# Performance work log

Measured on AMD Instinct MI355X. Metric: run time of the kernel, lower is better.

Reference implementation:

```python
import jax, jax.numpy as jnp
import numpy as np

D_MODEL = 1024
NHEAD = 16
HEAD_DIM = D_MODEL // NHEAD
NEG = -1e9
LN_EPS = 1e-5


def setup_inputs() -> dict:
    key = jax.random.key(0)
    ks = jax.random.split(key, 12)
    B, S, D = 2, 2048, D_MODEL
    scale = 1.0 / np.sqrt(D)
    inp = {
        "x": jax.random.normal(ks[0], (B, S, D), jnp.float32),
        "mask": jax.random.randint(ks[1], (B, S), 0, 2, jnp.int32),
        "wq": jax.random.normal(ks[2], (D, D), jnp.float32) * scale,
        "bq": jnp.zeros((D,), jnp.float32),
        "wk": jax.random.normal(ks[3], (D, D), jnp.float32) * scale,
        "bk": jnp.zeros((D,), jnp.float32),
        "wv": jax.random.normal(ks[4], (D, D), jnp.float32) * scale,
        "bv": jnp.zeros((D,), jnp.float32),
        "wo": jax.random.normal(ks[5], (D, D), jnp.float32) * scale,
        "bo": jnp.zeros((D,), jnp.float32),
        "attn_bias": jax.random.normal(ks[6], (1, NHEAD, 1, 1), jnp.float32) * 0.02,
        "ln_g": jnp.ones((D,), jnp.float32),
        "ln_b": jnp.zeros((D,), jnp.float32),
    }
    return inp


def _layer_norm(x, g, b):
    mu = jnp.mean(x, axis=-1, keepdims=True)
    var = jnp.var(x, axis=-1, keepdims=True)
    return (x - mu) * jax.lax.rsqrt(var + LN_EPS) * g + b


def reference(x, mask, wq, bq, wk, bk, wv, bv, wo, bo, attn_bias, ln_g, ln_b):
    B, S, D = x.shape
    H, Hd = NHEAD, HEAD_DIM
    # QKV projections -> [B, H, S, Hd]
    q = (x @ wq + bq).reshape(B, S, H, Hd).transpose(0, 2, 1, 3)
    k = (x @ wk + bk).reshape(B, S, H, Hd).transpose(0, 2, 1, 3)
    v = (x @ wv + bv).reshape(B, S, H, Hd).transpose(0, 2, 1, 3)
    # Scores [B, H, S, S] with per-head scalar bias
    scores = jnp.einsum("bhsd,bhtd->bhst", q, k) / jnp.sqrt(jnp.float32(Hd))
    scores = scores + attn_bias
    # mask [B,S] -> [B,1,1,S]; masked_fill where mask == 0
    m = (mask[:, None, None, :] == 0)
    scores = jnp.where(m, jnp.float32(NEG), scores)
    attn = jax.nn.softmax(scores, axis=-1)  # dropout = identity (eval)
    out = jnp.einsum("bhst,bhtd->bhsd", attn, v)
    out = out.transpose(0, 2, 1, 3).reshape(B, S, D)
    out = out @ wo + bo
    return _layer_norm(x + out, ln_g, ln_b)
```

## Files before the change

kernel.cpp:

```cpp
#include <hip/hip_runtime.h>

typedef __attribute__((ext_vector_type(8))) short short8;
typedef __attribute__((ext_vector_type(4))) float f32x4;
typedef __attribute__((ext_vector_type(16))) float f32x16;
typedef __attribute__((ext_vector_type(4))) unsigned short us4;

#define DEV __device__ __forceinline__

#define GLD16(gp, lp) __builtin_amdgcn_global_load_lds( \
    (const __attribute__((address_space(1))) void*)(gp), \
    (__attribute__((address_space(3))) void*)(lp), 16, 0, 0)

DEV unsigned short f2bf(float f) {
    union { float f; unsigned u; } v; v.f = f;
    unsigned r = v.u + 0x7fffu + ((v.u >> 16) & 1u);
    return (unsigned short)(r >> 16);
}

DEV float bf2f(unsigned short u) {
    union { unsigned u; float f; } v; v.u = (unsigned)u << 16;
    return v.f;
}

DEV unsigned cvtpk(float lo, float hi) {
    unsigned r;
    asm("v_cvt_pk_bf16_f32 %0, %1, %2" : "=v"(r) : "v"(lo), "v"(hi));
    return r;
}

DEV float fexp2(float x) {
#if __has_builtin(__builtin_amdgcn_exp2f)
    return __builtin_amdgcn_exp2f(x);
#else
    return __expf(x * 0.69314718056f);
#endif
}

__global__ __launch_bounds__(256) void k_transw(const float* __restrict__ wq, const float* __restrict__ wk,
                                                const float* __restrict__ wv, const float* __restrict__ wo,
                                                unsigned short* __restrict__ wt) {
    __shared__ float tile[32][33];
    const int z = blockIdx.z;
    const float* src = (z == 0) ? wq : (z == 1) ? wk : (z == 2) ? wv : wo;
    unsigned short* dst = wt + (size_t)z * (1u << 20);
    const int n0 = blockIdx.x * 32, k0 = blockIdx.y * 32;
    const int tx = threadIdx.x, ty = threadIdx.y;
#pragma unroll
    for (int i = 0; i < 4; ++i)
        tile[ty + i * 8][tx] = src[(size_t)(k0 + ty + i * 8) * 1024 + n0 + tx];
    __syncthreads();
#pragma unroll
    for (int i = 0; i < 4; ++i)
        dst[(size_t)(n0 + ty + i * 8) * 1024 + k0 + tx] = f2bf(tile[tx][ty + i * 8]);
}

__global__ __launch_bounds__(256) void k_gemm_qkv(const float* __restrict__ X,
                                                  const unsigned short* __restrict__ Wt,
                                                  const float* __restrict__ bq,
                                                  const float* __restrict__ bk,
                                                  const float* __restrict__ bv,
                                                  const int* __restrict__ mask,
                                                  unsigned short* __restrict__ Qo,
                                                  unsigned short* __restrict__ Ko,
                                                  unsigned short* __restrict__ Vo,
                                                  float qscale) {
    __shared__ unsigned short lA[2][128 * 32];
    __shared__ unsigned short lB[2][3][64 * 32];
    const int m0 = blockIdx.y * 128, n0 = blockIdx.x * 64;
    const int tid = threadIdx.x;
    const int lane = tid & 63;
    const int w = tid >> 6, wm = w >> 1, wn = w & 1;

    const int arow0 = tid >> 2, acl = tid & 3;
    const int arow1 = (tid + 256) >> 2;
    const int brow = tid >> 2;
    const float* agp0 = X + (size_t)(m0 + arow0) * 1024 + acl * 8;
    const float* agp1 = X + (size_t)(m0 + arow1) * 1024 + acl * 8;
    const unsigned short* bgp[3];
#pragma unroll
    for (int z = 0; z < 3; ++z)
        bgp[z] = Wt + ((size_t)z << 20) + (size_t)(n0 + brow) * 1024 + acl * 8;
    const int apc0 = ((arow0 << 2) | (acl ^ ((arow0 >> 1) & 3))) * 8;
    const int apc1 = ((arow1 << 2) | (acl ^ ((arow1 >> 1) & 3))) * 8;
    const int bpc  = ((brow  << 2) | (acl ^ ((brow  >> 1) & 3))) * 8;

    int ach[4], bch[2];
#pragma unroll
    for (int mt = 0; mt < 4; ++mt) {
        int row = wm * 64 + mt * 16 + (lane & 15);
        ach[mt] = ((row << 2) | ((lane >> 4) ^ ((row >> 1) & 3))) * 8;
    }
#pragma unroll
    for (int nt = 0; nt < 2; ++nt) {
        int row = wn * 32 + nt * 16 + (lane & 15);
        bch[nt] = ((row << 2) | ((lane >> 4) ^ ((row >> 1) & 3))) * 8;
    }

    f32x4 acc[3][4][2] = {};
    float4 ra0l = *(const float4*)agp0, ra0h = *(const float4*)(agp0 + 4);
    float4 ra1l = *(const float4*)agp1, ra1h = *(const float4*)(agp1 + 4);
    short8 rb[3];
#pragma unroll
    for (int z = 0; z < 3; ++z) rb[z] = *(const short8*)bgp[z];

    for (int t = 0; t < 32; ++t) {
        unsigned short* sA = lA[t & 1];
        union { unsigned u[4]; short8 s8; } p0, p1;
        p0.u[0] = cvtpk(ra0l.x, ra0l.y); p0.u[1] = cvtpk(ra0l.z, ra0l.w);
        p0.u[2] = cvtpk(ra0h.x, ra0h.y); p0.u[3] = cvtpk(ra0h.z, ra0h.w);
        p1.u[0] = cvtpk(ra1l.x, ra1l.y); p1.u[1] = cvtpk(ra1l.z, ra1l.w);
        p1.u[2] = cvtpk(ra1h.x, ra1h.y); p1.u[3] = cvtpk(ra1h.z, ra1h.w);
        *(short8*)(sA + apc0) = p0.s8;
        *(short8*)(sA + apc1) = p1.s8;
#pragma unroll
        for (int z = 0; z < 3; ++z)
            *(short8*)(lB[t & 1][z] + bpc) = rb[z];
        if (t < 31) {
            ra0l = *(const float4*)(agp0 + (t + 1) * 32);
            ra0h = *(const float4*)(agp0 + (t + 1) * 32 + 4);
            ra1l = *(const float4*)(agp1 + (t + 1) * 32);
            ra1h = *(const float4*)(agp1 + (t + 1) * 32 + 4);
#pragma unroll
            for (int z = 0; z < 3; ++z) rb[z] = *(const short8*)(bgp[z] + (t + 1) * 32);
        }
        __syncthreads();
        short8 af[4], bf[3][2];
#pragma unroll
        for (int mt = 0; mt < 4; ++mt) af[mt] = *(const short8*)(sA + ach[mt]);
#pragma unroll
        for (int z = 0; z < 3; ++z)
#pragma unroll
            for (int nt = 0; nt < 2; ++nt) bf[z][nt] = *(const short8*)(lB[t & 1][z] + bch[nt]);
#pragma unroll
        for (int z = 0; z < 3; ++z)
#pragma unroll
            for (int mt = 0; mt < 4; ++mt)
#pragma unroll
                for (int nt = 0; nt < 2; ++nt)
                    acc[z][mt][nt] = __builtin_amdgcn_mfma_f32_16x16x32_bf16(af[mt], bf[z][nt], acc[z][mt][nt], 0, 0, 0);
    }

#pragma unroll
    for (int z = 0; z < 3; ++z) {
        const float* bias = (z == 0) ? bq : (z == 1) ? bk : bv;
        const float scl = (z == 0) ? qscale : 1.0f;
        unsigned short* outp = (z == 0) ? Qo : (z == 1) ? Ko : Vo;
#pragma unroll
        for (int nt = 0; nt < 2; ++nt) {
            const int col = n0 + wn * 32 + nt * 16 + (lane & 15);
            const float bvv = bias[col];
            const int h = col >> 6, hd = col & 63;
#pragma unroll
            for (int mt = 0; mt < 4; ++mt) {
#pragma unroll
                for (int r = 0; r < 4; ++r) {
                    const int row = m0 + wm * 64 + mt * 16 + (lane >> 4) * 4 + r;
                    const int b = row >> 11, s = row & 2047;
                    float v = (acc[z][mt][nt][r] + bvv) * scl;
                    if (z == 2) {
                        v *= (mask[(size_t)b * 2048 + s] ? 1.0f : 0.0f);
                        outp[(size_t)((b * 16 + h) * 64 + hd) * 2048 + s] = f2bf(v);
                    } else {
                        outp[(size_t)((b * 16 + h) * 2048 + s) * 64 + hd] = f2bf(v);
                    }
                }
            }
        }
    }
}

__global__ __launch_bounds__(256) void k_gemm_o(const unsigned short* __restrict__ A,
                                                const unsigned short* __restrict__ Wt,
                                                const float* __restrict__ bias,
                                                unsigned short* __restrict__ out) {
    __shared__ unsigned short lA[2][128 * 32];
    __shared__ unsigned short lB[2][64 * 32];
    const int m0 = blockIdx.y * 128, n0 = blockIdx.x * 64;
    const int tid = threadIdx.x;
    const int lane = tid & 63;
    const int w = tid >> 6, wm = w >> 1, wn = w & 1;

    const int arow0 = tid >> 2, acl = tid & 3;
    const int arow1 = (tid + 256) >> 2;
    const int brow = tid >> 2;
    const unsigned short* agp0 = A + (size_t)(m0 + arow0) * 1024 + acl * 8;
    const unsigned short* agp1 = A + (size_t)(m0 + arow1) * 1024 + acl * 8;
    const unsigned short* bgp  = Wt + (size_t)(n0 + brow) * 1024 + acl * 8;
    const int apc0 = ((arow0 << 2) | (acl ^ ((arow0 >> 1) & 3))) * 8;
    const int apc1 = ((arow1 << 2) | (acl ^ ((arow1 >> 1) & 3))) * 8;
    const int bpc  = ((brow  << 2) | (acl ^ ((brow  >> 1) & 3))) * 8;

    int ach[4], bch[2];
#pragma unroll
    for (int mt = 0; mt < 4; ++mt) {
        int row = wm * 64 + mt * 16 + (lane & 15);
        ach[mt] = ((row << 2) | ((lane >> 4) ^ ((row >> 1) & 3))) * 8;
    }
#pragma unroll
    for (int nt = 0; nt < 2; ++nt) {
        int row = wn * 32 + nt * 16 + (lane & 15);
        bch[nt] = ((row << 2) | ((lane >> 4) ^ ((row >> 1) & 3))) * 8;
    }

    f32x4 acc[4][2] = {};
    short8 ra0 = *(const short8*)agp0;
    short8 ra1 = *(const short8*)agp1;
    short8 rb0 = *(const short8*)bgp;

    for (int t = 0; t < 32; ++t) {
        unsigned short* sA = lA[t & 1];
        unsigned short* sB = lB[t & 1];
        *(short8*)(sA + apc0) = ra0;
        *(short8*)(sA + apc1) = ra1;
        *(short8*)(sB + bpc)  = rb0;
        if (t < 31) {
            ra0 = *(const short8*)(agp0 + (t + 1) * 32);
            ra1 = *(const short8*)(agp1 + (t + 1) * 32);
            rb0 = *(const short8*)(bgp  + (t + 1) * 32);
        }
        __syncthreads();
        short8 af[4], bf[2];
#pragma unroll
        for (int mt = 0; mt < 4; ++mt) af[mt] = *(const short8*)(sA + ach[mt]);
#pragma unroll
        for (int nt = 0; nt < 2; ++nt) bf[nt] = *(const short8*)(sB + bch[nt]);
#pragma unroll
        for (int mt = 0; mt < 4; ++mt)
#pragma unroll
            for (int nt = 0; nt < 2; ++nt)
                acc[mt][nt] = __builtin_amdgcn_mfma_f32_16x16x32_bf16(af[mt], bf[nt], acc[mt][nt], 0, 0, 0);
    }

#pragma unroll
    for (int nt = 0; nt < 2; ++nt) {
        const int col = n0 + wn * 32 + nt * 16 + (lane & 15);
        const float bv = bias[col];
#pragma unroll
        for (int mt = 0; mt < 4; ++mt)
#pragma unroll
            for (int r = 0; r < 4; ++r) {
                const int row = m0 + wm * 64 + mt * 16 + (lane >> 4) * 4 + r;
                out[(size_t)row * 1024 + col] = f2bf(acc[mt][nt][r] + bv);
            }
    }
}

__global__ __launch_bounds__(256, 2) void k_attn(const unsigned short* __restrict__ Qb,
                                                 const unsigned short* __restrict__ Kb,
                                                 const unsigned short* __restrict__ Vt,
                                                 const int* __restrict__ mask,
                                                 unsigned short* __restrict__ po0,
                                                 unsigned short* __restrict__ po1,
                                                 float* __restrict__ lp0,
                                                 float* __restrict__ lp1) {
    __shared__ unsigned short ksm[2 * 4096];
    __shared__ unsigned short vsm[2 * 4096];
    __shared__ unsigned short mv[1024];
    const int id = blockIdx.x;
    const int xcd = id & 7, slot = id >> 3;
    const int half = slot & 1, qt = (slot >> 1) & 7, bh = xcd * 4 + (slot >> 4);
    const int b = bh >> 4, h = bh & 15;
    const int tid = threadIdx.x, l = tid & 63, w = tid >> 6;
    const int q = l & 31, hi = l >> 5;

    {
        int4 m = ((const int4*)(mask + b * 2048 + half * 1024))[tid];
        us4 mb = { (unsigned short)(m.x ? 0x3F80 : 0), (unsigned short)(m.y ? 0x3F80 : 0),
                   (unsigned short)(m.z ? 0x3F80 : 0), (unsigned short)(m.w ? 0x3F80 : 0) };
        ((us4*)mv)[tid] = mb;
    }
    asm volatile("s_waitcnt lgkmcnt(0)" ::: "memory");

    const size_t bhS = (size_t)bh * 2048;
    const unsigned short* Kbh = Kb + (bhS + half * 1024) * 64;
    const unsigned short* Vbh = Vt + (size_t)bh * 64 * 2048;
    const int q0 = qt * 256 + w * 64;

    const int srow = l >> 3;
    const int sxor = 8 * ((l & 7) ^ ((l >> 3) & 7));
    const unsigned short* Ksrc = Kbh + (size_t)(w * 16 + srow) * 64 + sxor;
    const unsigned short* Vsrc = Vbh + (size_t)(w * 16 + srow) * 2048 + half * 1024 + sxor;
    unsigned short* lk0 = ksm + w * 1024;
    unsigned short* lv0 = vsm + w * 1024;

#define STAGE(kt_, buf_) { \
    const unsigned short* gk = Ksrc + (size_t)(kt_) * 4096; \
    const unsigned short* gv = Vsrc + (kt_) * 64; \
    unsigned short* lk = lk0 + (buf_) * 4096; \
    unsigned short* lv = lv0 + (buf_) * 4096; \
    GLD16(gk, lk); GLD16(gk + 512, lk + 512); \
    GLD16(gv, lv); GLD16(gv + 16384, lv + 512); }

    int kro[2][4], vro[2][2][2];
#pragma unroll
    for (int sub = 0; sub < 2; ++sub) {
#pragma unroll
        for (int db = 0; db < 4; ++db) {
            int key = q + sub * 32;
            kro[sub][db] = key * 128 + ((db * 32 + hi * 16) ^ ((key & 7) << 4));
        }
#pragma unroll
        for (int kg = 0; kg < 2; ++kg)
#pragma unroll
            for (int dh = 0; dh < 2; ++dh) {
                int row = q + dh * 32;
                vro[sub][kg][dh] = row * 128 + ((sub * 64 + kg * 32 + hi * 16) ^ ((row & 7) << 4));
            }
    }

    short8 qfA[4], qfB[4];
#pragma unroll
    for (int db = 0; db < 4; ++db) {
        qfA[db] = *(const short8*)(Qb + (bhS + q0 + q) * 64 + db * 16 + hi * 8);
        qfB[db] = *(const short8*)(Qb + (bhS + q0 + 32 + q) * 64 + db * 16 + hi * 8);
    }

    f32x16 o00 = {}, o01 = {}, o10 = {}, o11 = {}, ol0 = {}, ol1 = {};

    STAGE(0, 0);

    for (int kt = 0; kt < 16; ++kt) {
        const int cur = kt & 1;
        if (kt < 15) {
            STAGE(kt + 1, cur ^ 1);
            asm volatile("s_waitcnt vmcnt(4)" ::: "memory");
        } else {
            asm volatile("s_waitcnt vmcnt(0)" ::: "memory");
        }
        __builtin_amdgcn_s_barrier();
        __builtin_amdgcn_sched_barrier(0);
        const char* kb = (const char*)(ksm + cur * 4096);
        const char* vb = (const char*)(vsm + cur * 4096);
#pragma unroll
        for (int sub = 0; sub < 2; ++sub) {
            short8 kf0 = *(const short8*)(kb + kro[sub][0]);
            short8 kf1 = *(const short8*)(kb + kro[sub][1]);
            short8 kf2 = *(const short8*)(kb + kro[sub][2]);
            short8 kf3 = *(const short8*)(kb + kro[sub][3]);
            f32x16 sa0 = {}, sa1 = {};
            __builtin_amdgcn_s_setprio(1);
            sa0 = __builtin_amdgcn_mfma_f32_32x32x16_bf16(kf0, qfA[0], sa0, 0, 0, 0);
            sa1 = __builtin_amdgcn_mfma_f32_32x32x16_bf16(kf0, qfB[0], sa1, 0, 0, 0);
            sa0 = __builtin_amdgcn_mfma_f32_32x32x16_bf16(kf1, qfA[1], sa0, 0, 0, 0);
            sa1 = __builtin_amdgcn_mfma_f32_32x32x16_bf16(kf1, qfB[1], sa1, 0, 0, 0);
            sa0 = __builtin_amdgcn_mfma_f32_32x32x16_bf16(kf2, qfA[2], sa0, 0, 0, 0);
            sa1 = __builtin_amdgcn_mfma_f32_32x32x16_bf16(kf2, qfB[2], sa1, 0, 0, 0);
            sa0 = __builtin_amdgcn_mfma_f32_32x32x16_bf16(kf3, qfA[3], sa0, 0, 0, 0);
            sa1 = __builtin_amdgcn_mfma_f32_32x32x16_bf16(kf3, qfB[3], sa1, 0, 0, 0);
            __builtin_amdgcn_s_setprio(0);
            union { unsigned u[4]; short8 s8; } afA[2], afB[2];
            {
                float p[16];
#pragma unroll
                for (int r = 0; r < 16; ++r) p[r] = fexp2(sa0[r]);
#pragma unroll
                for (int kg = 0; kg < 2; ++kg) {
                    unsigned P0 = cvtpk(p[kg * 8 + 0], p[kg * 8 + 1]);
                    unsigned P1 = cvtpk(p[kg * 8 + 2], p[kg * 8 + 3]);
                    unsigned P2 = cvtpk(p[kg * 8 + 4], p[kg * 8 + 5]);
                    unsigned P3 = cvtpk(p[kg * 8 + 6], p[kg * 8 + 7]);
                    asm("v_permlane32_swap_b32 %0, %1" : "+v"(P0), "+v"(P2));
                    asm("v_permlane32_swap_b32 %0, %1" : "+v"(P1), "+v"(P3));
                    afA[kg].u[0] = P0; afA[kg].u[1] = P1; afA[kg].u[2] = P2; afA[kg].u[3] = P3;
                }
            }
            {
                float p[16];
#pragma unroll
                for (int r = 0; r < 16; ++r) p[r] = fexp2(sa1[r]);
#pragma unroll
                for (int kg = 0; kg < 2; ++kg) {
                    unsigned P0 = cvtpk(p[kg * 8 + 0], p[kg * 8 + 1]);
                    unsigned P1 = cvtpk(p[kg * 8 + 2], p[kg * 8 + 3]);
                    unsigned P2 = cvtpk(p[kg * 8 + 4], p[kg * 8 + 5]);
                    unsigned P3 = cvtpk(p[kg * 8 + 6], p[kg * 8 + 7]);
                    asm("v_permlane32_swap_b32 %0, %1" : "+v"(P0), "+v"(P2));
                    asm("v_permlane32_swap_b32 %0, %1" : "+v"(P1), "+v"(P3));
                    afB[kg].u[0] = P0; afB[kg].u[1] = P1; afB[kg].u[2] = P2; afB[kg].u[3] = P3;
                }
            }
#pragma unroll
            for (int kg = 0; kg < 2; ++kg) {
                short8 vf0 = *(const short8*)(vb + vro[sub][kg][0]);
                short8 vf1 = *(const short8*)(vb + vro[sub][kg][1]);
                short8 mfr = *(const short8*)(mv + kt * 64 + sub * 32 + kg * 16 + hi * 8);
                __builtin_amdgcn_s_setprio(1);
                o00 = __builtin_amdgcn_mfma_f32_32x32x16_bf16(afA[kg].s8, vf0, o00, 0, 0, 0);
                o01 = __builtin_amdgcn_mfma_f32_32x32x16_bf16(afA[kg].s8, vf1, o01, 0, 0, 0);
                o10 = __builtin_amdgcn_mfma_f32_32x32x16_bf16(afB[kg].s8, vf0, o10, 0, 0, 0);
                o11 = __builtin_amdgcn_mfma_f32_32x32x16_bf16(afB[kg].s8, vf1, o11, 0, 0, 0);
                ol0 = __builtin_amdgcn_mfma_f32_32x32x16_bf16(afA[kg].s8, mfr, ol0, 0, 0, 0);
                ol1 = __builtin_amdgcn_mfma_f32_32x32x16_bf16(afB[kg].s8, mfr, ol1, 0, 0, 0);
                __builtin_amdgcn_s_setprio(0);
            }
        }
        __builtin_amdgcn_sched_barrier(0);
        if (kt < 15) __builtin_amdgcn_s_barrier();
    }
#undef STAGE

    float* lpx = half ? lp1 : lp0;
    if (q == 0) {
#pragma unroll
        for (int r = 0; r < 16; ++r) {
            int crow = (r & 3) + 8 * (r >> 2) + 4 * hi;
            lpx[bhS + q0 + crow] = ol0[r];
            lpx[bhS + q0 + 32 + crow] = ol1[r];
        }
    }
    unsigned short* popA = (half ? po1 : po0) + ((size_t)b * 2048 + q0) * 1024 + h * 64 + q;
    unsigned short* popB = popA + (size_t)32 * 1024;
#pragma unroll
    for (int r = 0; r < 16; ++r) {
        int qrow = (r & 3) + 8 * (r >> 2) + 4 * hi;
        popA[(size_t)qrow * 1024] = f2bf(o00[r]);
        popA[(size_t)qrow * 1024 + 32] = f2bf(o01[r]);
        popB[(size_t)qrow * 1024] = f2bf(o10[r]);
        popB[(size_t)qrow * 1024 + 32] = f2bf(o11[r]);
    }
}

__global__ __launch_bounds__(256) void k_comb(const unsigned short* __restrict__ po0,
                                              const unsigned short* __restrict__ po1,
                                              const float* __restrict__ lp0,
                                              const float* __restrict__ lp1,
                                              unsigned short* __restrict__ ao) {
    const int idx8 = blockIdx.x * 256 + threadIdx.x;
    const int e = idx8 * 8;
    const int row = e >> 10, c = e & 1023;
    const int h = c >> 6, b = row >> 11, s = row & 2047;
    const size_t li = ((size_t)(b * 16 + h) << 11) + s;
    const float rinv = __builtin_amdgcn_rcpf(lp0[li] + lp1[li]);
    short8 a0 = ((const short8*)po0)[idx8];
    short8 a1 = ((const short8*)po1)[idx8];
    short8 o;
#pragma unroll
    for (int j = 0; j < 8; ++j)
        o[j] = (short)f2bf((bf2f((unsigned short)a0[j]) + bf2f((unsigned short)a1[j])) * rinv);
    ((short8*)ao)[idx8] = o;
}

__global__ __launch_bounds__(256) void k_ln(const float* __restrict__ x, const unsigned short* __restrict__ op,
                                            const float* __restrict__ g, const float* __restrict__ be,
                                            float* __restrict__ out) {
    const int row = blockIdx.x, tid = threadIdx.x;
    const float4 xv = ((const float4*)(x + (size_t)row * 1024))[tid];
    const us4 ov = ((const us4*)(op + (size_t)row * 1024))[tid];
    float4 v = { xv.x + bf2f(ov.x), xv.y + bf2f(ov.y), xv.z + bf2f(ov.z), xv.w + bf2f(ov.w) };
    float sum = v.x + v.y + v.z + v.w;
    float ss = v.x * v.x + v.y * v.y + v.z * v.z + v.w * v.w;
#pragma unroll
    for (int xm = 1; xm < 64; xm <<= 1) {
        sum += __shfl_xor(sum, xm, 64);
        ss += __shfl_xor(ss, xm, 64);
    }
    __shared__ float red[8];
    const int lane = tid & 63, w = tid >> 6;
    if (lane == 0) { red[w] = sum; red[4 + w] = ss; }
    __syncthreads();
    sum = red[0] + red[1] + red[2] + red[3];
    ss = red[4] + red[5] + red[6] + red[7];
    const float mu = sum * (1.0f / 1024.0f);
    const float rstd = rsqrtf(ss * (1.0f / 1024.0f) - mu * mu + 1e-5f);
    const float4 gv = ((const float4*)g)[tid];
    const float4 bv = ((const float4*)be)[tid];
    float4 o = { (v.x - mu) * rstd * gv.x + bv.x, (v.y - mu) * rstd * gv.y + bv.y,
                 (v.z - mu) * rstd * gv.z + bv.z, (v.w - mu) * rstd * gv.w + bv.w };
    ((float4*)(out + (size_t)row * 1024))[tid] = o;
}

extern "C" void kernel_launch(void* const* d_in, const int* in_sizes, int n_in,
                              void* d_out, int out_size, void* d_ws, size_t ws_size,
                              hipStream_t stream) {
    const float* x        = (const float*)d_in[0];
    const int*   mask     = (const int*)d_in[1];
    const float* wq       = (const float*)d_in[2];
    const float* bq       = (const float*)d_in[3];
    const float* wk       = (const float*)d_in[4];
    const float* bk       = (const float*)d_in[5];
    const float* wv       = (const float*)d_in[6];
    const float* bv       = (const float*)d_in[7];
    const float* wo       = (const float*)d_in[8];
    const float* bo       = (const float*)d_in[9];
    const float* ln_g     = (const float*)d_in[11];
    const float* ln_b     = (const float*)d_in[12];

    char* ws = (char*)d_ws;
    unsigned short* po0 = (unsigned short*)(ws);
    unsigned short* wt  = (unsigned short*)(ws + (8ll  << 20));
    unsigned short* qb  = (unsigned short*)(ws + (16ll << 20));
    unsigned short* kb  = (unsigned short*)(ws + (24ll << 20));
    unsigned short* vtb = (unsigned short*)(ws + (32ll << 20));
    unsigned short* po1 = (unsigned short*)(ws + (40ll << 20));
    float*          lp0 = (float*)(ws + (48ll << 20));
    float*          lp1 = (float*)(ws + (48ll << 20) + (256ll << 10));
    unsigned short* ao  = qb;
    unsigned short* opj = kb;

    const float qscale = 0.125f * 1.44269504f;

    k_transw<<<dim3(32, 32, 4), dim3(32, 8), 0, stream>>>(wq, wk, wv, wo, wt);
    k_gemm_qkv<<<dim3(16, 32), 256, 0, stream>>>(x, wt, bq, bk, bv, mask, qb, kb, vtb, qscale);
    k_attn<<<512, 256, 0, stream>>>(qb, kb, vtb, mask, po0, po1, lp0, lp1);
    k_comb<<<2048, 256, 0, stream>>>(po0, po1, lp0, lp1, ao);
    k_gemm_o<<<dim3(16, 32), 256, 0, stream>>>(ao, wt + (3u << 20), bo, opj);
    k_ln<<<4096, 256, 0, stream>>>(x, opj, ln_g, ln_b, (float*)d_out);
}
```

Measured before the change: 124.0 us.

## Pre-convert X to bf16, fuse split-attention combine into O-projection, swizzle GEMM blocks

New measurement: 132.1 us. 6.6% more time.

```diff
diff --git a/kernel.cpp b/kernel.cpp
--- a/kernel.cpp
+++ b/kernel.cpp
@@ -34,6 +34,14 @@
 #else
     return __expf(x * 0.69314718056f);
 #endif
+}
+
+__global__ __launch_bounds__(256) void k_convert(const float* __restrict__ x,
+                                                 unsigned short* __restrict__ xb) {
+    int i = blockIdx.x * 256 + threadIdx.x;
+    float4 v = ((const float4*)x)[i];
+    us4 o = { f2bf(v.x), f2bf(v.y), f2bf(v.z), f2bf(v.w) };
+    ((us4*)xb)[i] = o;
 }
 
 __global__ __launch_bounds__(256) void k_transw(const float* __restrict__ wq, const float* __restrict__ wk,
@@ -54,7 +62,7 @@
         dst[(size_t)(n0 + ty + i * 8) * 1024 + k0 + tx] = f2bf(tile[tx][ty + i * 8]);
 }
 
-__global__ __launch_bounds__(256) void k_gemm_qkv(const float* __restrict__ X,
+__global__ __launch_bounds__(256) void k_gemm_qkv(const unsigned short* __restrict__ A,
                                                   const unsigned short* __restrict__ Wt,
                                                   const float* __restrict__ bq,
                                                   const float* __restrict__ bk,
@@ -66,7 +74,9 @@
                                                   float qscale) {
     __shared__ unsigned short lA[2][128 * 32];
     __shared__ unsigned short lB[2][3][64 * 32];
-    const int m0 = blockIdx.y * 128, n0 = blockIdx.x * 64;
+    const int id = blockIdx.x;
+    const int m0 = ((id & 7) * 4 + ((id >> 3) & 3)) * 128;
+    const int n0 = (id >> 5) * 64;
     const int tid = threadIdx.x;
     const int lane = tid & 63;
     const int w = tid >> 6, wm = w >> 1, wn = w & 1;
@@ -74,8 +84,8 @@
     const int arow0 = tid >> 2, acl = tid & 3;
     const int arow1 = (tid + 256) >> 2;
     const int brow = tid >> 2;
-    const float* agp0 = X + (size_t)(m0 + arow0) * 1024 + acl * 8;
-    const float* agp1 = X + (size_t)(m0 + arow1) * 1024 + acl * 8;
+    const unsigned short* agp0 = A + (size_t)(m0 + arow0) * 1024 + acl * 8;
+    const unsigned short* agp1 = A + (size_t)(m0 + arow1) * 1024 + acl * 8;
     const unsigned short* bgp[3];
 #pragma unroll
     for (int z = 0; z < 3; ++z)
@@ -97,29 +107,22 @@
     }
 
     f32x4 acc[3][4][2] = {};
-    float4 ra0l = *(const float4*)agp0, ra0h = *(const float4*)(agp0 + 4);
-    float4 ra1l = *(const float4*)agp1, ra1h = *(const float4*)(agp1 + 4);
+    short8 ra0 = *(const short8*)agp0;
+    short8 ra1 = *(const short8*)agp1;
     short8 rb[3];
 #pragma unroll
     for (int z = 0; z < 3; ++z) rb[z] = *(const short8*)bgp[z];
 
     for (int t = 0; t < 32; ++t) {
         unsigned short* sA = lA[t & 1];
-        union { unsigned u[4]; short8 s8; } p0, p1;
-        p0.u[0] = cvtpk(ra0l.x, ra0l.y); p0.u[1] = cvtpk(ra0l.z, ra0l.w);
-        p0.u[2] = cvtpk(ra0h.x, ra0h.y); p0.u[3] = cvtpk(ra0h.z, ra0h.w);
-        p1.u[0] = cvtpk(ra1l.x, ra1l.y); p1.u[1] = cvtpk(ra1l.z, ra1l.w);
-        p1.u[2] = cvtpk(ra1h.x, ra1h.y); p1.u[3] = cvtpk(ra1h.z, ra1h.w);
-        *(short8*)(sA + apc0) = p0.s8;
-        *(short8*)(sA + apc1) = p1.s8;
+        *(short8*)(sA + apc0) = ra0;
+        *(short8*)(sA + apc1) = ra1;
 #pragma unroll
         for (int z = 0; z < 3; ++z)
             *(short8*)(lB[t & 1][z] + bpc) = rb[z];
         if (t < 31) {
-            ra0l = *(const float4*)(agp0 + (t + 1) * 32);
-            ra0h = *(const float4*)(agp0 + (t + 1) * 32 + 4);
-            ra1l = *(const float4*)(agp1 + (t + 1) * 32);
-            ra1h = *(const float4*)(agp1 + (t + 1) * 32 + 4);
+            ra0 = *(const short8*)(agp0 + (t + 1) * 32);
+            ra1 = *(const short8*)(agp1 + (t + 1) * 32);
 #pragma unroll
             for (int z = 0; z < 3; ++z) rb[z] = *(const short8*)(bgp[z] + (t + 1) * 32);
         }
@@ -169,22 +172,42 @@
     }
 }
 
-__global__ __launch_bounds__(256) void k_gemm_o(const unsigned short* __restrict__ A,
+__global__ __launch_bounds__(256) void k_rinv(const float* __restrict__ lp0,
+                                              const float* __restrict__ lp1,
+                                              float* __restrict__ rv) {
+    int i = blockIdx.x * 256 + threadIdx.x;
+    float4 a = ((const float4*)lp0)[i];
+    float4 b = ((const float4*)lp1)[i];
+    float4 o = { __builtin_amdgcn_rcpf(a.x + b.x), __builtin_amdgcn_rcpf(a.y + b.y),
+                 __builtin_amdgcn_rcpf(a.z + b.z), __builtin_amdgcn_rcpf(a.w + b.w) };
+    ((float4*)rv)[i] = o;
+}
+
+__global__ __launch_bounds__(256) void k_gemm_o(const unsigned short* __restrict__ po0,
+                                                const unsigned short* __restrict__ po1,
+                                                const float* __restrict__ rinv,
                                                 const unsigned short* __restrict__ Wt,
                                                 const float* __restrict__ bias,
                                                 unsigned short* __restrict__ out) {
     __shared__ unsigned short lA[2][128 * 32];
     __shared__ unsigned short lB[2][64 * 32];
-    const int m0 = blockIdx.y * 128, n0 = blockIdx.x * 64;
+    const int id = blockIdx.x;
+    const int m0 = ((id & 7) * 4 + ((id >> 3) & 3)) * 128;
+    const int n0 = (id >> 5) * 64;
     const int tid = threadIdx.x;
     const int lane = tid & 63;
     const int w = tid >> 6, wm = w >> 1, wn = w & 1;
 
     const int arow0 = tid >> 2, acl = tid & 3;
-    const int arow1 = (tid + 256) >> 2;
+    const int arow1 = arow0 + 64;
     const int brow = tid >> 2;
-    const unsigned short* agp0 = A + (size_t)(m0 + arow0) * 1024 + acl * 8;
-    const unsigned short* agp1 = A + (size_t)(m0 + arow1) * 1024 + acl * 8;
+    const int row0 = m0 + arow0, row1 = m0 + arow1;
+    const int bb = row0 >> 11;
+    const int s0 = row0 & 2047, s1 = row1 & 2047;
+    const unsigned short* pg00 = po0 + (size_t)row0 * 1024 + acl * 8;
+    const unsigned short* pg10 = po1 + (size_t)row0 * 1024 + acl * 8;
+    const unsigned short* pg01 = po0 + (size_t)row1 * 1024 + acl * 8;
+    const unsigned short* pg11 = po1 + (size_t)row1 * 1024 + acl * 8;
     const unsigned short* bgp  = Wt + (size_t)(n0 + brow) * 1024 + acl * 8;
     const int apc0 = ((arow0 << 2) | (acl ^ ((arow0 >> 1) & 3))) * 8;
     const int apc1 = ((arow1 << 2) | (acl ^ ((arow1 >> 1) & 3))) * 8;
@@ -203,20 +226,38 @@
     }
 
     f32x4 acc[4][2] = {};
-    short8 ra0 = *(const short8*)agp0;
-    short8 ra1 = *(const short8*)agp1;
+    short8 q00 = *(const short8*)pg00, q10 = *(const short8*)pg10;
+    short8 q01 = *(const short8*)pg01, q11 = *(const short8*)pg11;
     short8 rb0 = *(const short8*)bgp;
+    int h = (acl * 8) >> 6;
+    float ri0 = rinv[((size_t)(bb * 16 + h) << 11) + s0];
+    float ri1 = rinv[((size_t)(bb * 16 + h) << 11) + s1];
 
     for (int t = 0; t < 32; ++t) {
         unsigned short* sA = lA[t & 1];
         unsigned short* sB = lB[t & 1];
-        *(short8*)(sA + apc0) = ra0;
-        *(short8*)(sA + apc1) = ra1;
+        union { unsigned u[4]; short8 s8; } n0_, n1_;
+#pragma unroll
+        for (int jj = 0; jj < 4; ++jj) {
+            float f0 = (bf2f((unsigned short)q00[jj * 2]) + bf2f((unsigned short)q10[jj * 2])) * ri0;
+            float f1 = (bf2f((unsigned short)q00[jj * 2 + 1]) + bf2f((unsigned short)q10[jj * 2 + 1])) * ri0;
+            n0_.u[jj] = cvtpk(f0, f1);
+            float g0 = (bf2f((unsigned short)q01[jj * 2]) + bf2f((unsigned short)q11[jj * 2])) * ri1;
+            float g1 = (bf2f((unsigned short)q01[jj * 2 + 1]) + bf2f((unsigned short)q11[jj * 2 + 1])) * ri1;
+            n1_.u[jj] = cvtpk(g0, g1);
+        }
+        *(short8*)(sA + apc0) = n0_.s8;
+        *(short8*)(sA + apc1) = n1_.s8;
         *(short8*)(sB + bpc)  = rb0;
         if (t < 31) {
-            ra0 = *(const short8*)(agp0 + (t + 1) * 32);
-            ra1 = *(const short8*)(agp1 + (t + 1) * 32);
+            q00 = *(const short8*)(pg00 + (t + 1) * 32);
+            q10 = *(const short8*)(pg10 + (t + 1) * 32);
+            q01 = *(const short8*)(pg01 + (t + 1) * 32);
+            q11 = *(const short8*)(pg11 + (t + 1) * 32);
             rb0 = *(const short8*)(bgp  + (t + 1) * 32);
+            h = ((t + 1) * 32 + acl * 8) >> 6;
+            ri0 = rinv[((size_t)(bb * 16 + h) << 11) + s0];
+            ri1 = rinv[((size_t)(bb * 16 + h) << 11) + s1];
         }
         __syncthreads();
         short8 af[4], bf[2];
@@ -420,26 +461,6 @@
     }
 }
 
-__global__ __launch_bounds__(256) void k_comb(const unsigned short* __restrict__ po0,
-                                              const unsigned short* __restrict__ po1,
-                                              const float* __restrict__ lp0,
-                                              const float* __restrict__ lp1,
-                                              unsigned short* __restrict__ ao) {
-    const int idx8 = blockIdx.x * 256 + threadIdx.x;
-    const int e = idx8 * 8;
-    const int row = e >> 10, c = e & 1023;
-    const int h = c >> 6, b = row >> 11, s = row & 2047;
-    const size_t li = ((size_t)(b * 16 + h) << 11) + s;
-    const float rinv = __builtin_amdgcn_rcpf(lp0[li] + lp1[li]);
-    short8 a0 = ((const short8*)po0)[idx8];
-    short8 a1 = ((const short8*)po1)[idx8];
-    short8 o;
-#pragma unroll
-    for (int j = 0; j < 8; ++j)
-        o[j] = (short)f2bf((bf2f((unsigned short)a0[j]) + bf2f((unsigned short)a1[j])) * rinv);
-    ((short8*)ao)[idx8] = o;
-}
-
 __global__ __launch_bounds__(256) void k_ln(const float* __restrict__ x, const unsigned short* __restrict__ op,
                                             const float* __restrict__ g, const float* __restrict__ be,
                                             float* __restrict__ out) {
@@ -486,7 +507,7 @@
     const float* ln_b     = (const float*)d_in[12];
 
     char* ws = (char*)d_ws;
-    unsigned short* po0 = (unsigned short*)(ws);
+    unsigned short* xb  = (unsigned short*)(ws);
     unsigned short* wt  = (unsigned short*)(ws + (8ll  << 20));
     unsigned short* qb  = (unsigned short*)(ws + (16ll << 20));
     unsigned short* kb  = (unsigned short*)(ws + (24ll << 20));
@@ -494,15 +515,17 @@
     unsigned short* po1 = (unsigned short*)(ws + (40ll << 20));
     float*          lp0 = (float*)(ws + (48ll << 20));
     float*          lp1 = (float*)(ws + (48ll << 20) + (256ll << 10));
-    unsigned short* ao  = qb;
+    float*          rv  = (float*)(ws + (48ll << 20) + (512ll << 10));
+    unsigned short* po0 = xb;
     unsigned short* opj = kb;
 
     const float qscale = 0.125f * 1.44269504f;
 
+    k_convert<<<4096, 256, 0, stream>>>(x, xb);
     k_transw<<<dim3(32, 32, 4), dim3(32, 8), 0, stream>>>(wq, wk, wv, wo, wt);
-    k_gemm_qkv<<<dim3(16, 32), 256, 0, stream>>>(x, wt, bq, bk, bv, mask, qb, kb, vtb, qscale);
+    k_gemm_qkv<<<512, 256, 0, stream>>>(xb, wt, bq, bk, bv, mask, qb, kb, vtb, qscale);
     k_attn<<<512, 256, 0, stream>>>(qb, kb, vtb, mask, po0, po1, lp0, lp1);
-    k_comb<<<2048, 256, 0, stream>>>(po0, po1, lp0, lp1, ao);
-    k_gemm_o<<<dim3(16, 32), 256, 0, stream>>>(ao, wt + (3u << 20), bo, opj);
+    k_rinv<<<64, 256, 0, stream>>>(lp0, lp1, rv);
+    k_gemm_o<<<512, 256, 0, stream>>>(po0, po1, rv, wt + (3u << 20), bo, opj);
     k_ln<<<4096, 256, 0, stream>>>(x, opj, ln_g, ln_b, (float*)d_out);
 }
```
